# Performance work log

Measured on AMD Instinct MI355X. Metric: run time of the kernel, lower is better.

Reference implementation:

```python
import jax, jax.numpy as jnp
import numpy as np

T = 36  # num_frames


def box_cxcywh_to_xyxy(b):
    cx, cy, w, h = jnp.split(b, 4, axis=-1)
    return jnp.concatenate([cx - 0.5 * w, cy - 0.5 * h, cx + 0.5 * w, cy + 0.5 * h], axis=-1)


def multi_iou(b1, b2):
    # b1: [Q,1,T,4], b2: [1,N,T,4], xyxy -> iou [Q,N,T]
    lt = jnp.maximum(b1[..., :2], b2[..., :2])
    rb = jnp.minimum(b1[..., 2:], b2[..., 2:])
    wh = jnp.clip(rb - lt, 0.0)
    inter = wh[..., 0] * wh[..., 1]
    a1 = (b1[..., 2] - b1[..., 0]) * (b1[..., 3] - b1[..., 1])
    a2 = (b2[..., 2] - b2[..., 0]) * (b2[..., 3] - b2[..., 1])
    union = a1 + a2 - inter
    return inter / union


def setup_inputs() -> dict:
    key = jax.random.key(0)
    k1, k2, k3, k4, k5, k6 = jax.random.split(key, 6)
    Q, N, C = 2048, 128, 42
    return {
        "pred_logits": jax.random.normal(k1, (T * Q, C), dtype=jnp.float32),
        "pred_boxes": jax.random.uniform(k2, (T * Q, 4), dtype=jnp.float32),
        "tgt_labels": jax.random.randint(k3, (N * T,), 0, C - 1),
        "tgt_boxes": jax.random.uniform(k4, (N * T, 4), dtype=jnp.float32),
        "tgt_valid": jax.random.randint(k5, (N * T,), 0, 2, dtype=jnp.int32),
        "tgt_original_valid": jax.random.randint(k6, (N * T,), 0, 2, dtype=jnp.int32),
    }


def reference(pred_logits, pred_boxes, tgt_labels, tgt_boxes, tgt_valid, tgt_original_valid):
    # Cost-matrix computation of SoftMaxHungarianMatcher (cost_class=cost_bbox=cost_giou=1,
    # use_giou=False, use_l1_distance_sum=False). The scipy linear_sum_assignment step is
    # CPU-serial / non-tensor and excluded; output is the [Q,N] cost fed to it.
    C = pred_logits.shape[-1]
    Q = pred_logits.shape[0] // T
    N = tgt_labels.shape[0] // T
    num_classes = C - 1  # background index

    probs = jax.nn.softmax(pred_logits, axis=-1).reshape(T, Q, C).transpose(1, 0, 2)  # [Q,T,C]
    boxes = pred_boxes.reshape(T, Q, 4).transpose(1, 0, 2)                            # [Q,T,4]
    tboxes = tgt_boxes.reshape(N, T, 4)
    valid = tgt_valid.reshape(N, T).astype(probs.dtype)                               # [N,T]
    ovalid = tgt_original_valid.reshape(N, T)
    ids = jnp.where(ovalid == 0, num_classes, tgt_labels.reshape(N, T))               # [N,T]

    denom = valid.sum(-1)  # [N] (per-instance count of valid frames)

    # class cost: -mean_t p(q, t, ids[n,t]) over valid frames
    gathered = probs[:, jnp.arange(T)[None, :], ids]                                  # [Q,N,T]
    class_cost = -(gathered * valid).sum(-1) / denom                                  # [Q,N]

    # bbox L1 cost: mean over (valid frames, 4 coords)
    l1 = jnp.abs(boxes[:, None] - tboxes[None]).mean(-1)                              # [Q,N,T]
    bbox_cost = (l1 * valid).sum(-1) / denom                                          # [Q,N]

    # IoU cost: -mean_t iou over valid frames
    iou = multi_iou(box_cxcywh_to_xyxy(boxes)[:, None], box_cxcywh_to_xyxy(tboxes)[None])
    iou_cost = -(iou * valid).sum(-1) / denom                                         # [Q,N]

    return class_cost + bbox_cost + iou_cost
```

## Files before the change

kernel.cpp:

```cpp
#include <hip/hip_runtime.h>
#include <hip/hip_bf16.h>


constexpr int T = 36;
constexpr int Q = 2048;
constexpr int C = 42;
constexpr int N = 128;

__global__ __launch_bounds__(256) void softmax_transpose_kernel(
    const float* __restrict__ logits, __hip_bfloat16* __restrict__ P2) {
  constexpr int QB = 64;

  __shared__ float tile[QB * C];
  __shared__ float s_rinv[QB];

  const int t = blockIdx.y;
  const int q0 = blockIdx.x * QB;
  const int tid = threadIdx.x;

  {
    const float4* src = (const float4*)(logits + ((size_t)t * Q + q0) * C);
    float4* dst = (float4*)tile;
    for (int i = tid; i < QB * C / 4; i += 256) {
      float4 v = src[i];
      float4 e;
      e.x = __expf(v.x);
      e.y = __expf(v.y);
      e.z = __expf(v.z);
      e.w = __expf(v.w);
      dst[i] = e;
    }
  }
  __syncthreads();

  {
    const int row = tid >> 2;
    const int part = tid & 3;
    const int c0 = (part < 2) ? part * 11 : 22 + (part - 2) * 10;
    const int c1 = (part < 2) ? c0 + 11 : c0 + 10;
    float s = 0.f;
    for (int c = c0; c < c1; ++c) s += tile[row * C + c];
    s += __shfl_xor(s, 1);
    s += __shfl_xor(s, 2);
    if (part == 0) s_rinv[row] = __builtin_amdgcn_rcpf(s);
  }
  __syncthreads();

  for (int i = tid; i < QB * C / 2; i += 256) {
    int c = i >> 5;
    int r2 = i & 31;
    float v0 = tile[(2 * r2) * C + c] * s_rinv[2 * r2];
    float v1 = tile[(2 * r2 + 1) * C + c] * s_rinv[2 * r2 + 1];
    __hip_bfloat162 pk;
    pk.x = __float2bfloat16(v0);
    pk.y = __float2bfloat16(v1);
    *(__hip_bfloat162*)(P2 + (size_t)(t * C + c) * Q + q0 + 2 * r2) = pk;
  }
}

__global__ __launch_bounds__(512) void cost_kernel(
    const __hip_bfloat16* __restrict__ P2, const float* __restrict__ pred_boxes,
    const int* __restrict__ labels, const float* __restrict__ tboxes,
    const int* __restrict__ valid, const int* __restrict__ ovalid,
    float* __restrict__ out) {
  constexpr int NB = 4;
  constexpr int RS = NB + 1;

  const int q0 = blockIdx.x * 64;
  const int n0 = blockIdx.y * NB;
  const int tid = threadIdx.x;
  const int lane = tid & 63;
  const int sub = (tid >> 6) & 3;
  const int half = tid >> 8;
  const int q = q0 + lane;

  __shared__ float4 s_tb[NB * T];
  __shared__ int s_idv[NB * T];
  __shared__ float s_rden[NB];
  __shared__ float s_res[2 * 64 * RS];

  for (int i = tid; i < NB * T; i += 512) {
    int n = n0 + i / T;
    int t = i % T;
    int g = n * T + t;
    s_idv[i] = ((ovalid[g] == 0) ? (C - 1) : labels[g]) | (valid[g] << 8);
    s_tb[i] = ((const float4*)tboxes)[g];
  }
  if (tid < NB) {
    int n = n0 + tid;
    int s = 0;
    for (int t = 0; t < T; ++t) s += valid[n * T + t];
    s_rden[tid] = 1.f / (float)s;
  }
  __syncthreads();

  float acc = 0.f;
  const __hip_bfloat16* probs_base = P2 + q;
  const int t_begin = half * (T / 2);
  const int t_end = t_begin + (T / 2);

  for (int t = t_begin; t < t_end; ++t) {
    int pk = s_idv[sub * T + t];
    if (pk & 0x100) {
      float4 pb = ((const float4*)pred_boxes)[t * Q + q];
      float4 tb = s_tb[sub * T + t];
      int id = pk & 0xff;
      float p = __bfloat162float(probs_base[(size_t)(t * C + id) * Q]);

      float l1 = 0.25f * (fabsf(pb.x - tb.x) + fabsf(pb.y - tb.y) +
                          fabsf(pb.z - tb.z) + fabsf(pb.w - tb.w));
      float px1 = pb.x - 0.5f * pb.z, py1 = pb.y - 0.5f * pb.w;
      float px2 = pb.x + 0.5f * pb.z, py2 = pb.y + 0.5f * pb.w;
      float tx1 = tb.x - 0.5f * tb.z, ty1 = tb.y - 0.5f * tb.w;
      float tx2 = tb.x + 0.5f * tb.z, ty2 = tb.y + 0.5f * tb.w;
      float iw = fmaxf(fminf(px2, tx2) - fmaxf(px1, tx1), 0.f);
      float ih = fmaxf(fminf(py2, ty2) - fmaxf(py1, ty1), 0.f);
      float inter = iw * ih;
      float uni = pb.z * pb.w + tb.z * tb.w - inter;
      acc += l1 - p - inter * __builtin_amdgcn_rcpf(uni);
    }
  }

  s_res[half * (64 * RS) + lane * RS + sub] = acc;
  __syncthreads();
  if (half == 0) {
    float tot = (acc + s_res[64 * RS + lane * RS + sub]) * s_rden[sub];
    s_res[lane * RS + sub] = tot;
  }
  __syncthreads();

  if (tid < 64) {
    float4 o;
    o.x = s_res[tid * RS + 0];
    o.y = s_res[tid * RS + 1];
    o.z = s_res[tid * RS + 2];
    o.w = s_res[tid * RS + 3];
    *(float4*)(out + (size_t)(q0 + tid) * N + n0) = o;
  }
}

extern "C" void kernel_launch(void* const* d_in, const int* in_sizes, int n_in,
                              void* d_out, int out_size, void* d_ws, size_t ws_size,
                              hipStream_t stream) {
  const float* logits = (const float*)d_in[0];
  const float* pboxes = (const float*)d_in[1];
  const int* labels = (const int*)d_in[2];
  const float* tboxes = (const float*)d_in[3];
  const int* valid = (const int*)d_in[4];
  const int* ovalid = (const int*)d_in[5];
  float* out = (float*)d_out;

  __hip_bfloat16* P2 = (__hip_bfloat16*)d_ws;

  dim3 g1(Q / 64, T);
  softmax_transpose_kernel<<<g1, 256, 0, stream>>>(logits, P2);

  dim3 g2(Q / 64, N / 4);
  cost_kernel<<<g2, 512, 0, stream>>>(P2, pboxes, labels, tboxes, valid, ovalid, out);
}
```

Baseline: 81.51 us.

## Fuse softmax and cost computation into a single kernel with LDS-resident probabilities

Replaces the two-kernel pipeline (softmax to a bf16 transposed workspace, then cost kernel) with one kernel per 8-query block that computes the softmax for all 36 frames into shared memory and then evaluates all 128 targets. This removes the intermediate global round trip and the second launch. Validity handling becomes branchless: each frame is multiplied by its valid flag and the valid count is accumulated in the loop. Probabilities now stay fp32 instead of bf16. The block needs about 48 KB of LDS and 1024 threads, which limits occupancy, and grid size falls to 256 blocks.

```diff
diff --git a/kernel.cpp b/kernel.cpp
--- a/kernel.cpp
+++ b/kernel.cpp
@@ -6,136 +6,111 @@
 constexpr int Q = 2048;
 constexpr int C = 42;
 constexpr int N = 128;
+constexpr int QB = 8;
 
-__global__ __launch_bounds__(256) void softmax_transpose_kernel(
-    const float* __restrict__ logits, __hip_bfloat16* __restrict__ P2) {
-  constexpr int QB = 64;
+__global__ __launch_bounds__(1024) void fused_kernel(
+    const float* __restrict__ logits, const float* __restrict__ pboxes,
+    const int* __restrict__ labels, const float* __restrict__ tboxes,
+    const int* __restrict__ valid, const int* __restrict__ ovalid,
+    float* __restrict__ out) {
+  __shared__ float s_p[T * QB * C];
+  __shared__ unsigned int s_idv[N * 9];
+  __shared__ float s_out[QB * N];
 
-  __shared__ float tile[QB * C];
-  __shared__ float s_rinv[QB];
+  const int tid = threadIdx.x;
+  const int q0 = blockIdx.x * QB;
 
-  const int t = blockIdx.y;
-  const int q0 = blockIdx.x * QB;
-  const int tid = threadIdx.x;
+  for (int i = tid; i < N * 9; i += 1024) {
+    int n = i / 9;
+    int t4 = (i - n * 9) * 4;
+    unsigned int w = 0;
+#pragma unroll
+    for (int k = 0; k < 4; ++k) {
+      int g = n * T + t4 + k;
+      unsigned int id =
+          (ovalid[g] == 0) ? (unsigned)(C - 1) : (unsigned)labels[g];
+      w |= (id | (valid[g] ? 64u : 0u)) << (8 * k);
+    }
+    s_idv[i] = w;
+  }
 
-  {
-    const float4* src = (const float4*)(logits + ((size_t)t * Q + q0) * C);
-    float4* dst = (float4*)tile;
-    for (int i = tid; i < QB * C / 4; i += 256) {
-      float4 v = src[i];
-      float4 e;
-      e.x = __expf(v.x);
-      e.y = __expf(v.y);
-      e.z = __expf(v.z);
-      e.w = __expf(v.w);
-      dst[i] = e;
-    }
+  for (int i = tid; i < T * 84; i += 1024) {
+    int t = i / 84;
+    int idx = i - t * 84;
+    float4 v = ((const float4*)(logits + ((size_t)t * Q + q0) * C))[idx];
+    float4 e;
+    e.x = __expf(v.x);
+    e.y = __expf(v.y);
+    e.z = __expf(v.z);
+    e.w = __expf(v.w);
+    ((float4*)s_p)[t * 84 + idx] = e;
   }
   __syncthreads();
 
-  {
-    const int row = tid >> 2;
-    const int part = tid & 3;
-    const int c0 = (part < 2) ? part * 11 : 22 + (part - 2) * 10;
-    const int c1 = (part < 2) ? c0 + 11 : c0 + 10;
+  if (tid < T * QB * 2) {
+    const int r = tid >> 1;
+    const int half = tid & 1;
+    float* rowp = s_p + r * C + half * 21;
+    float e[21];
     float s = 0.f;
-    for (int c = c0; c < c1; ++c) s += tile[row * C + c];
+#pragma unroll
+    for (int k = 0; k < 21; ++k) {
+      e[k] = rowp[k];
+      s += e[k];
+    }
     s += __shfl_xor(s, 1);
-    s += __shfl_xor(s, 2);
-    if (part == 0) s_rinv[row] = __builtin_amdgcn_rcpf(s);
+    float rs = __builtin_amdgcn_rcpf(s);
+#pragma unroll
+    for (int k = 0; k < 21; ++k) rowp[k] = e[k] * rs;
   }
   __syncthreads();
 
-  for (int i = tid; i < QB * C / 2; i += 256) {
-    int c = i >> 5;
-    int r2 = i & 31;
-    float v0 = tile[(2 * r2) * C + c] * s_rinv[2 * r2];
-    float v1 = tile[(2 * r2 + 1) * C + c] * s_rinv[2 * r2 + 1];
-    __hip_bfloat162 pk;
-    pk.x = __float2bfloat16(v0);
-    pk.y = __float2bfloat16(v1);
-    *(__hip_bfloat162*)(P2 + (size_t)(t * C + c) * Q + q0 + 2 * r2) = pk;
-  }
-}
+  const int qL = tid & 7;
+  const int n = tid >> 3;
+  const int q = q0 + qL;
 
-__global__ __launch_bounds__(512) void cost_kernel(
-    const __hip_bfloat16* __restrict__ P2, const float* __restrict__ pred_boxes,
-    const int* __restrict__ labels, const float* __restrict__ tboxes,
-    const int* __restrict__ valid, const int* __restrict__ ovalid,
-    float* __restrict__ out) {
-  constexpr int NB = 4;
-  constexpr int RS = NB + 1;
+  float acc = 0.f, sumv = 0.f;
+  const unsigned int* idvp = s_idv + n * 9;
+  const float* prow = s_p + qL * C;
 
-  const int q0 = blockIdx.x * 64;
-  const int n0 = blockIdx.y * NB;
-  const int tid = threadIdx.x;
-  const int lane = tid & 63;
-  const int sub = (tid >> 6) & 3;
-  const int half = tid >> 8;
-  const int q = q0 + lane;
+  for (int tw = 0; tw < 9; ++tw) {
+    unsigned int w = idvp[tw];
+#pragma unroll
+    for (int k = 0; k < 4; ++k) {
+      const int t = tw * 4 + k;
+      unsigned int b = (w >> (8 * k)) & 0xFFu;
+      float vf = (float)(b >> 6);
+      int id = (int)(b & 63u);
+      float p = prow[(t * QB) * C + id];
+      float4 pb = ((const float4*)pboxes)[t * Q + q];
+      float4 tb = ((const float4*)tboxes)[n * T + t];
 
-  __shared__ float4 s_tb[NB * T];
-  __shared__ int s_idv[NB * T];
-  __shared__ float s_rden[NB];
-  __shared__ float s_res[2 * 64 * RS];
+      float px1 = fmaf(-0.5f, pb.z, pb.x), py1 = fmaf(-0.5f, pb.w, pb.y);
+      float px2 = fmaf(0.5f, pb.z, pb.x), py2 = fmaf(0.5f, pb.w, pb.y);
+      float tx1 = fmaf(-0.5f, tb.z, tb.x), ty1 = fmaf(-0.5f, tb.w, tb.y);
+      float tx2 = fmaf(0.5f, tb.z, tb.x), ty2 = fmaf(0.5f, tb.w, tb.y);
 
-  for (int i = tid; i < NB * T; i += 512) {
-    int n = n0 + i / T;
-    int t = i % T;
-    int g = n * T + t;
-    s_idv[i] = ((ovalid[g] == 0) ? (C - 1) : labels[g]) | (valid[g] << 8);
-    s_tb[i] = ((const float4*)tboxes)[g];
-  }
-  if (tid < NB) {
-    int n = n0 + tid;
-    int s = 0;
-    for (int t = 0; t < T; ++t) s += valid[n * T + t];
-    s_rden[tid] = 1.f / (float)s;
-  }
-  __syncthreads();
-
-  float acc = 0.f;
-  const __hip_bfloat16* probs_base = P2 + q;
-  const int t_begin = half * (T / 2);
-  const int t_end = t_begin + (T / 2);
-
-  for (int t = t_begin; t < t_end; ++t) {
-    int pk = s_idv[sub * T + t];
-    if (pk & 0x100) {
-      float4 pb = ((const float4*)pred_boxes)[t * Q + q];
-      float4 tb = s_tb[sub * T + t];
-      int id = pk & 0xff;
-      float p = __bfloat162float(probs_base[(size_t)(t * C + id) * Q]);
-
-      float l1 = 0.25f * (fabsf(pb.x - tb.x) + fabsf(pb.y - tb.y) +
-                          fabsf(pb.z - tb.z) + fabsf(pb.w - tb.w));
-      float px1 = pb.x - 0.5f * pb.z, py1 = pb.y - 0.5f * pb.w;
-      float px2 = pb.x + 0.5f * pb.z, py2 = pb.y + 0.5f * pb.w;
-      float tx1 = tb.x - 0.5f * tb.z, ty1 = tb.y - 0.5f * tb.w;
-      float tx2 = tb.x + 0.5f * tb.z, ty2 = tb.y + 0.5f * tb.w;
+      float s4 = fabsf(pb.x - tb.x) + fabsf(pb.y - tb.y) +
+                 fabsf(pb.z - tb.z) + fabsf(pb.w - tb.w);
       float iw = fmaxf(fminf(px2, tx2) - fmaxf(px1, tx1), 0.f);
       float ih = fmaxf(fminf(py2, ty2) - fmaxf(py1, ty1), 0.f);
       float inter = iw * ih;
-      float uni = pb.z * pb.w + tb.z * tb.w - inter;
-      acc += l1 - p - inter * __builtin_amdgcn_rcpf(uni);
+      float uni = fmaf(tb.z, tb.w, pb.z * pb.w) - inter;
+      float iou = inter * __builtin_amdgcn_rcpf(uni);
+      float term = fmaf(0.25f, s4, -p) - iou;
+      acc = fmaf(vf, term, acc);
+      sumv += vf;
     }
   }
 
-  s_res[half * (64 * RS) + lane * RS + sub] = acc;
-  __syncthreads();
-  if (half == 0) {
-    float tot = (acc + s_res[64 * RS + lane * RS + sub]) * s_rden[sub];
-    s_res[lane * RS + sub] = tot;
-  }
+  s_out[qL * N + n] = acc * __builtin_amdgcn_rcpf(sumv);
   __syncthreads();
 
-  if (tid < 64) {
-    float4 o;
-    o.x = s_res[tid * RS + 0];
-    o.y = s_res[tid * RS + 1];
-    o.z = s_res[tid * RS + 2];
-    o.w = s_res[tid * RS + 3];
-    *(float4*)(out + (size_t)(q0 + tid) * N + n0) = o;
+  if (tid < 256) {
+    int qr = tid >> 5;
+    int nf = tid & 31;
+    float4 v = ((const float4*)s_out)[qr * 32 + nf];
+    ((float4*)out)[(size_t)(q0 + qr) * (N / 4) + nf] = v;
   }
 }
 
@@ -150,11 +125,6 @@
   const int* ovalid = (const int*)d_in[5];
   float* out = (float*)d_out;
 
-  __hip_bfloat16* P2 = (__hip_bfloat16*)d_ws;
-
-  dim3 g1(Q / 64, T);
-  softmax_transpose_kernel<<<g1, 256, 0, stream>>>(logits, P2);
-
-  dim3 g2(Q / 64, N / 4);
-  cost_kernel<<<g2, 512, 0, stream>>>(P2, pboxes, labels, tboxes, valid, ovalid, out);
+  fused_kernel<<<dim3(Q / QB), 1024, 0, stream>>>(logits, pboxes, labels,
+                                                  tboxes, valid, ovalid, out);
 }
```

Result: slower. 84.55 us (+3.7%).
